# Kernel tuning notes

Measured on AMD Instinct MI355X. Metric: run time of the kernel, lower is better.

## Reference

```python
import jax, jax.numpy as jnp
import numpy as np
import math

B, S, D = 16, 512, 1024
H, L = 16, 4
DH = D // H
EPS = 1e-5


def _layernorm(x, w, b):
    mu = jnp.mean(x, axis=-1, keepdims=True)
    var = jnp.mean(jnp.square(x - mu), axis=-1, keepdims=True)
    return (x - mu) / jnp.sqrt(var + EPS) * w + b


def _pos_encoding(s, d):
    pos = jnp.arange(s, dtype=jnp.float32)[:, None]                      # [s,1]
    div = jnp.exp(jnp.arange(0, d, 2, dtype=jnp.float32) * (-math.log(10000.0) / d))
    ang = pos * div[None, :]                                             # [s,d/2]
    return jnp.stack([jnp.sin(ang), jnp.cos(ang)], axis=-1).reshape(s, d)  # interleave sin/cos


def _attention_layer(x, Wq, bq, Wv, bv, Wo, bo, gamma, ln_w, ln_b, mask):
    bs, s, d = x.shape
    # q_linear == k_linear (kq_same=True)
    q = (x @ Wq.T + bq).reshape(bs, s, H, DH).transpose(0, 2, 1, 3)      # [b,h,s,dh]
    k = q
    v = (x @ Wv.T + bv).reshape(bs, s, H, DH).transpose(0, 2, 1, 3)

    scores = jnp.einsum('bhqd,bhkd->bhqk', q, k) / math.sqrt(DH)         # [b,h,s,s]

    # distance-decay modulation (dist_scores is detached in the original)
    p = jax.nn.softmax(jnp.where(mask, scores, -1e32), axis=-1)
    distcum = jnp.cumsum(p, axis=-1)
    disttot = jnp.sum(p, axis=-1, keepdims=True)
    idx = jnp.arange(s, dtype=jnp.float32)
    pos_eff = jnp.abs(idx[None, :] - idx[:, None])[None, None, :, :]     # |i-j|
    dist = jnp.sqrt(jnp.maximum((disttot - distcum) * pos_eff, 0.0))
    dist = jax.lax.stop_gradient(dist)

    g = -jnp.abs(gamma)[None, :, None, None]                             # [1,h,1,1]
    total_effect = jnp.clip(jnp.exp(dist * g), 1e-5, 1e5)
    scores = scores * total_effect

    scores = jnp.where(mask, scores, -1e32)
    attn = jax.nn.softmax(scores, axis=-1)
    attn = jnp.where(mask, attn, 0.0)

    # maxout=True (peek_cur=False): clamp(1/max, max=5)
    scale = jnp.minimum(1.0 / jnp.max(attn, axis=-1, keepdims=True), 5.0)
    attn = attn * scale

    out = jnp.einsum('bhqk,bhkd->bhqd', attn, v)                         # [b,h,s,dh]
    out = out.transpose(0, 2, 1, 3).reshape(bs, s, d)
    out = out @ Wo.T + bo

    # eval mode: dropout = identity; residual + layernorm
    return _layernorm(x + out, ln_w, ln_b), attn


def reference(x, lens, Wq, bq, Wv, bv, Wo, bo, gammas, ln_w, ln_b, fln_w, fln_b):
    del lens  # only used in training-mode random masking
    s = x.shape[1]
    q = x + _pos_encoding(s, D)[None, :, :]
    mask = jnp.tril(jnp.ones((s, s), dtype=bool), -1)[None, None, :, :]  # peek_cur=False
    scores = None
    for l in range(L):
        q, scores = _attention_layer(q, Wq[l], bq[l], Wv[l], bv[l], Wo[l], bo[l],
                                     gammas[l], ln_w[l], ln_b[l], mask)
    return _layernorm(q, fln_w, fln_b), scores


def setup_inputs() -> dict:
    key = jax.random.key(0)
    ks = jax.random.split(key, 8)
    wscale = 1.0 / math.sqrt(D)
    return {
        'x': jax.random.normal(ks[0], (B, S, D), dtype=jnp.float32),
        'lens': jax.random.randint(ks[1], (B,), 1, S),
        'Wq': jax.random.normal(ks[2], (L, D, D), dtype=jnp.float32) * wscale,
        'bq': jnp.zeros((L, D), dtype=jnp.float32),
        'Wv': jax.random.normal(ks[3], (L, D, D), dtype=jnp.float32) * wscale,
        'bv': jnp.zeros((L, D), dtype=jnp.float32),
        'Wo': jax.random.normal(ks[4], (L, D, D), dtype=jnp.float32) * wscale,
        'bo': jnp.zeros((L, D), dtype=jnp.float32),
        'gammas': jax.random.uniform(ks[5], (L, H), dtype=jnp.float32, minval=-1.7, maxval=1.7),
        'ln_w': jnp.ones((L, D), dtype=jnp.float32),
        'ln_b': jnp.zeros((L, D), dtype=jnp.float32),
        'fln_w': jnp.ones((D,), dtype=jnp.float32),
        'fln_b': jnp.zeros((D,), dtype=jnp.float32),
    }
```

## Files before the change

kernel.cpp:

```cpp
#include <hip/hip_runtime.h>
#include <hip/hip_bf16.h>

#define BB 16
#define SS 512
#define DD 1024
#define HH 16
#define LL 4
#define DHH 64
#define GK 1024

typedef __attribute__((ext_vector_type(8))) short short8;
typedef __attribute__((ext_vector_type(4))) float f32x4;

__device__ __forceinline__ unsigned short f2bf(float f) {
  union { float f; unsigned int u; } v; v.f = f;
  unsigned int r = v.u + 0x7FFFu + ((v.u >> 16) & 1u);
  return (unsigned short)(r >> 16);
}

__device__ __forceinline__ float wave_max(float v) {
#pragma unroll
  for (int off = 32; off > 0; off >>= 1) v = fmaxf(v, __shfl_xor(v, off));
  return v;
}
__device__ __forceinline__ float wave_sum(float v) {
#pragma unroll
  for (int off = 32; off > 0; off >>= 1) v += __shfl_xor(v, off);
  return v;
}
__device__ __forceinline__ float half_max(float v) {
#pragma unroll
  for (int off = 16; off > 0; off >>= 1) v = fmaxf(v, __shfl_xor(v, off));
  return v;
}
__device__ __forceinline__ float half_sum(float v) {
#pragma unroll
  for (int off = 16; off > 0; off >>= 1) v += __shfl_xor(v, off);
  return v;
}

__device__ __forceinline__ void gl16(const void* g, void* l) {
  __builtin_amdgcn_global_load_lds(
      (const __attribute__((address_space(1))) unsigned int*)(uintptr_t)g,
      (__attribute__((address_space(3))) unsigned int*)(unsigned int)(uintptr_t)l,
      16, 0, 0);
}

__global__ __launch_bounds__(256) void k_w2bf_all(
    const float* __restrict__ wq, const float* __restrict__ wv,
    const float* __restrict__ wo, unsigned short* __restrict__ oqv,
    unsigned short* __restrict__ oo) {
  size_t i4 = ((size_t)blockIdx.x * 256 + threadIdx.x) * 4;
  const size_t QV = (size_t)2 * LL * DD * DD;
  const float* src;
  unsigned short* dst;
  if (i4 < QV) {
    size_t l = i4 >> 21;
    size_t r = i4 & ((1u << 21) - 1);
    src = (r < (1u << 20)) ? wq + (l << 20) + r
                           : wv + (l << 20) + (r - (1u << 20));
    dst = oqv + i4;
  } else {
    size_t j = i4 - QV;
    src = wo + j;
    dst = oo + j;
  }
  float4 v = *(const float4*)src;
  uint2 pk;
  pk.x = (unsigned)f2bf(v.x) | ((unsigned)f2bf(v.y) << 16);
  pk.y = (unsigned)f2bf(v.z) | ((unsigned)f2bf(v.w) << 16);
  *(uint2*)dst = pk;
}

__global__ __launch_bounds__(256) void k_add_pe(const float* __restrict__ x,
                                                float* __restrict__ out,
                                                unsigned short* __restrict__ outb) {
  size_t i4 = ((size_t)blockIdx.x * 256 + threadIdx.x) * 4;
  int d0 = (int)(i4 & (DD - 1));
  int s = (int)((i4 >> 10) & (SS - 1));
  float4 xv = *(const float4*)(x + i4);
  int ip0 = d0 >> 1;
  float f0 = __expf((float)ip0 * -0.017988946039016f);
  float f1 = __expf((float)(ip0 + 1) * -0.017988946039016f);
  float s0v, c0v, s1v, c1v;
  __sincosf((float)s * f0, &s0v, &c0v);
  __sincosf((float)s * f1, &s1v, &c1v);
  float4 o;
  o.x = xv.x + s0v; o.y = xv.y + c0v; o.z = xv.z + s1v; o.w = xv.w + c1v;
  *(float4*)(out + i4) = o;
  uint2 pk;
  pk.x = (unsigned)f2bf(o.x) | ((unsigned)f2bf(o.y) << 16);
  pk.y = (unsigned)f2bf(o.z) | ((unsigned)f2bf(o.w) << 16);
  *(uint2*)(outb + i4) = pk;
}

template <int MODE>
__global__ __launch_bounds__(256) void k_gemm(
    const unsigned short* __restrict__ A, const unsigned short* __restrict__ W,
    const float* __restrict__ bias, const float* __restrict__ bias2,
    void* __restrict__ out, void* __restrict__ out2) {
  __shared__ unsigned short As[2][128 * 32];
  __shared__ unsigned short Bs[2][128 * 32];
  const int tid = threadIdx.x;
  const int lane = tid & 63;
  const int w = tid >> 6;
  const int wr = w >> 1, wc = w & 1;
  const int fr = lane & 15, fq = lane >> 4;

  int bid = blockIdx.x;
  const int cpx = gridDim.x >> 3;
  bid = (bid & 7) * cpx + (bid >> 3);
  const int bm = (bid & 63) * 128;
  const int bn = (bid >> 6) * 128;

  f32x4 acc[4][4] = {};

  const unsigned short* ga = A + (size_t)(bm + w * 16 + (lane >> 2)) * GK + (lane & 3) * 8;
  const unsigned short* gb = W + (size_t)(bn + w * 16 + (lane >> 2)) * GK + (lane & 3) * 8;

  auto STAGE = [&](int buf, int k0) {
    unsigned short* la = As[buf] + w * 512;
    unsigned short* lb = Bs[buf] + w * 512;
    gl16(ga + k0, la);
    gl16(ga + 64 * GK + k0, la + 2048);
    gl16(gb + k0, lb);
    gl16(gb + 64 * GK + k0, lb + 2048);
  };

  STAGE(0, 0);
  __syncthreads();
  int cur = 0;
  for (int k0 = 0; k0 < GK; k0 += 32) {
    if (k0 + 32 < GK) STAGE(cur ^ 1, k0 + 32);
    short8 af[4], bf[4];
#pragma unroll
    for (int m = 0; m < 4; ++m)
      af[m] = *(const short8*)(As[cur] + (wr * 64 + m * 16 + fr) * 32 + fq * 8);
#pragma unroll
    for (int n = 0; n < 4; ++n)
      bf[n] = *(const short8*)(Bs[cur] + (wc * 64 + n * 16 + fr) * 32 + fq * 8);
#pragma unroll
    for (int m = 0; m < 4; ++m)
#pragma unroll
      for (int n = 0; n < 4; ++n)
        acc[m][n] = __builtin_amdgcn_mfma_f32_16x16x32_bf16(af[m], bf[n], acc[m][n], 0, 0, 0);
    __syncthreads();
    cur ^= 1;
  }

#pragma unroll
  for (int m = 0; m < 4; ++m) {
    const int row0 = bm + wr * 64 + m * 16 + fq * 4;
#pragma unroll
    for (int n = 0; n < 4; ++n) {
      const int col = bn + wc * 64 + n * 16 + fr;
      if constexpr (MODE == 0) {
        const float bsv = bias[col];
        unsigned short* o = (unsigned short*)out;
#pragma unroll
        for (int r = 0; r < 4; ++r)
          o[(size_t)(row0 + r) * DD + col] = f2bf(acc[m][n][r] + bsv);
      } else if constexpr (MODE == 2) {
        const float bsv = bias[col];
        float* o = (float*)out;
#pragma unroll
        for (int r = 0; r < 4; ++r)
          o[(size_t)(row0 + r) * DD + col] = acc[m][n][r] + bsv;
      } else {
        if (col < DD) {
          const float bsv = bias[col];
          unsigned short* o = (unsigned short*)out;
#pragma unroll
          for (int r = 0; r < 4; ++r)
            o[(size_t)(row0 + r) * DD + col] = f2bf(acc[m][n][r] + bsv);
        } else {
          const int c2 = col - DD;
          const float bsv = bias2[c2];
          unsigned short* o = (unsigned short*)out2;
          const int bi = row0 >> 9, si = row0 & (SS - 1);
          uint2 pk;
          pk.x = (unsigned)f2bf(acc[m][n][0] + bsv) | ((unsigned)f2bf(acc[m][n][1] + bsv) << 16);
          pk.y = (unsigned)f2bf(acc[m][n][2] + bsv) | ((unsigned)f2bf(acc[m][n][3] + bsv) << 16);
          *(uint2*)(o + ((size_t)bi * DD + c2) * SS + si) = pk;
        }
      }
    }
  }
}

__global__ __launch_bounds__(512) void k_attn(
    const unsigned short* __restrict__ Q, const unsigned short* __restrict__ Vt,
    const float* __restrict__ gam, unsigned short* __restrict__ AO,
    float* __restrict__ scores_out) {
  __shared__ float sc_s[32][516];
  __shared__ unsigned short KV[64][72];

  const int tid = threadIdx.x;
  const int lane = tid & 63;
  const int w = tid >> 6;
  const int wr = w & 1;
  const int wc = w >> 1;
  const int fr = lane & 15, fq = lane >> 4;

  const int itile = 15 - (blockIdx.x >> 8);
  const int bh = blockIdx.x & 255;
  const int b = bh >> 4;
  const int h = bh & 15;
  const int i0 = itile * 32;
  const int njt = (itile + 2) >> 1;
  const int jcap = njt * 64;

  const unsigned short* Qb = Q + (size_t)b * SS * DD + h * DHH;
  const unsigned short* Vtb = Vt + ((size_t)b * DD + h * DHH) * SS;
  const float gneg = -fabsf(gam[h]);

  const int srow = tid >> 3;
  const int sdb = (tid & 7) * 8;

  const unsigned short* qrow = Qb + (size_t)(i0 + wr * 16 + fr) * DD;
  short8 a0 = *(const short8*)(qrow + fq * 8);
  short8 a1 = *(const short8*)(qrow + 32 + fq * 8);

  short8 kreg = *(const short8*)(Qb + (size_t)srow * DD + sdb);
  for (int jt = 0; jt < njt; ++jt) {
    *(short8*)&KV[srow][sdb] = kreg;
    const unsigned short* nsrc = (jt + 1 < njt)
        ? Qb + (size_t)((jt + 1) * 64 + srow) * DD + sdb
        : Vtb + (size_t)srow * SS + sdb;
    kreg = *(const short8*)nsrc;
    __syncthreads();

    short8 b0 = *(const short8*)&KV[wc * 16 + fr][fq * 8];
    short8 b1 = *(const short8*)&KV[wc * 16 + fr][32 + fq * 8];
    f32x4 s0 = {};
    s0 = __builtin_amdgcn_mfma_f32_16x16x32_bf16(a0, b0, s0, 0, 0, 0);
    s0 = __builtin_amdgcn_mfma_f32_16x16x32_bf16(a1, b1, s0, 0, 0, 0);

    const int j = jt * 64 + wc * 16 + fr;
#pragma unroll
    for (int r = 0; r < 4; ++r) {
      const int row = wr * 16 + fq * 4 + r;
      sc_s[row][j] = (j < i0 + row) ? s0[r] * 0.125f : -1e30f;
    }
    __syncthreads();
  }
  *(short8*)&KV[srow][sdb] = kreg;

  if (itile >= 8) {
    const int jb = lane << 3;
#pragma unroll 2
    for (int q = 0; q < 4; ++q) {
      const int r_i = w * 4 + q;
      const int gi = i0 + r_i;
      const float* rowp = &sc_s[r_i][0];
      float4 v0 = *(const float4*)(rowp + jb);
      float4 v1 = *(const float4*)(rowp + jb + 4);
      float sc[8] = {v0.x, v0.y, v0.z, v0.w, v1.x, v1.y, v1.z, v1.w};
#pragma unroll
      for (int c = 0; c < 8; ++c)
        if (jb + c >= jcap) sc[c] = -1e30f;

      float p[8];
      float lsum = 0.0f;
#pragma unroll
      for (int c = 0; c < 8; ++c) {
        p[c] = __expf(sc[c]);
        lsum += p[c];
      }

      float xs = lsum;
#pragma unroll
      for (int off = 1; off < 64; off <<= 1) {
        float y = __shfl_up(xs, off);
        if (lane >= off) xs += y;
      }
      const float tot = __shfl(xs, 63);
      const float inv = 1.0f / tot;
      float run = xs - lsum;

      float s2[8];
#pragma unroll
      for (int c = 0; c < 8; ++c) {
        run += p[c];
        float cum = run * inv;
        float dist = sqrtf(fmaxf((1.0f - cum) * (float)(gi - (jb + c)), 0.0f));
        float te = __expf(gneg * dist);
        te = fminf(fmaxf(te, 1e-5f), 1e5f);
        s2[c] = sc[c] * te;
      }

      float m2 = s2[0];
#pragma unroll
      for (int c = 1; c < 8; ++c) m2 = fmaxf(m2, s2[c]);
      m2 = wave_max(m2);
      float e[8];
      float lsum2 = 0.0f;
#pragma unroll
      for (int c = 0; c < 8; ++c) {
        e[c] = __expf(s2[c] - m2);
        lsum2 += e[c];
      }
      float tot2 = wave_sum(lsum2);
      float mult = fminf(tot2, 5.0f) / tot2;

      float av[8];
#pragma unroll
      for (int c = 0; c < 8; ++c) av[c] = (gi == 0) ? 0.0f : e[c] * mult;

      if (scores_out) {
        float* so = scores_out + ((size_t)(b * HH + h) * SS + gi) * SS + jb;
        *(float4*)(so) = make_float4(av[0], av[1], av[2], av[3]);
        *(float4*)(so + 4) = make_float4(av[4], av[5], av[6], av[7]);
      }

      short8 pk;
#pragma unroll
      for (int c = 0; c < 8; ++c) pk[c] = (short)f2bf(av[c]);
      *(short8*)((unsigned short*)&sc_s[r_i][0] + jb) = pk;
    }
  } else {
    const int half = lane >> 5;
    const int ll = lane & 31;
    const int jb = ll << 3;
    for (int q = 0; q < 2; ++q) {
      const int r_i = w * 4 + q * 2 + half;
      const int gi = i0 + r_i;
      const float* rowp = &sc_s[r_i][0];
      float4 v0 = *(const float4*)(rowp + jb);
      float4 v1 = *(const float4*)(rowp + jb + 4);
      float sc[8] = {v0.x, v0.y, v0.z, v0.w, v1.x, v1.y, v1.z, v1.w};
#pragma unroll
      for (int c = 0; c < 8; ++c)
        if (jb + c >= jcap) sc[c] = -1e30f;

      float p[8];
      float lsum = 0.0f;
#pragma unroll
      for (int c = 0; c < 8; ++c) {
        p[c] = __expf(sc[c]);
        lsum += p[c];
      }

      float xs = lsum;
#pragma unroll
      for (int off = 1; off < 32; off <<= 1) {
        float y = __shfl_up(xs, off, 32);
        if (ll >= off) xs += y;
      }
      const float tot = __shfl(xs, 31, 32);
      const float inv = 1.0f / tot;
      float run = xs - lsum;

      float s2[8];
#pragma unroll
      for (int c = 0; c < 8; ++c) {
        run += p[c];
        float cum = run * inv;
        float dist = sqrtf(fmaxf((1.0f - cum) * (float)(gi - (jb + c)), 0.0f));
        float te = __expf(gneg * dist);
        te = fminf(fmaxf(te, 1e-5f), 1e5f);
        s2[c] = sc[c] * te;
      }

      float m2 = s2[0];
#pragma unroll
      for (int c = 1; c < 8; ++c) m2 = fmaxf(m2, s2[c]);
      m2 = half_max(m2);
      float e[8];
      float lsum2 = 0.0f;
#pragma unroll
      for (int c = 0; c < 8; ++c) {
        e[c] = __expf(s2[c] - m2);
        lsum2 += e[c];
      }
      const float tot2 = half_sum(lsum2);
      const float mult = fminf(tot2, 5.0f) / tot2;

      float av[8];
#pragma unroll
      for (int c = 0; c < 8; ++c) av[c] = (gi == 0) ? 0.0f : e[c] * mult;

      if (scores_out) {
        float* so = scores_out + ((size_t)(b * HH + h) * SS + gi) * SS + jb;
        *(float4*)(so) = make_float4(av[0], av[1], av[2], av[3]);
        *(float4*)(so + 4) = make_float4(av[4], av[5], av[6], av[7]);
        *(float4*)(so + 256) = make_float4(0.f, 0.f, 0.f, 0.f);
        *(float4*)(so + 260) = make_float4(0.f, 0.f, 0.f, 0.f);
      }

      short8 pk;
#pragma unroll
      for (int c = 0; c < 8; ++c) pk[c] = (short)f2bf(av[c]);
      *(short8*)((unsigned short*)&sc_s[r_i][0] + jb) = pk;
    }
  }
  __syncthreads();

  short8 vreg;
  if (njt > 1) vreg = *(const short8*)(Vtb + (size_t)srow * SS + 64 + sdb);
  f32x4 o0 = {};
  for (int jt = 0; jt < njt; ++jt) {
    const unsigned short* arow = (const unsigned short*)&sc_s[wr * 16 + fr][0];
    short8 pa0 = *(const short8*)(arow + jt * 64 + fq * 8);
    short8 pa1 = *(const short8*)(arow + jt * 64 + 32 + fq * 8);
    short8 c0 = *(const short8*)&KV[wc * 16 + fr][fq * 8];
    short8 c1 = *(const short8*)&KV[wc * 16 + fr][32 + fq * 8];
    o0 = __builtin_amdgcn_mfma_f32_16x16x32_bf16(pa0, c0, o0, 0, 0, 0);
    o0 = __builtin_amdgcn_mfma_f32_16x16x32_bf16(pa1, c1, o0, 0, 0, 0);
    __syncthreads();
    if (jt + 1 < njt) {
      *(short8*)&KV[srow][sdb] = vreg;
      if (jt + 2 < njt) vreg = *(const short8*)(Vtb + (size_t)srow * SS + (jt + 2) * 64 + sdb);
      __syncthreads();
    }
  }

  {
    const int d = h * DHH + wc * 16 + fr;
#pragma unroll
    for (int r = 0; r < 4; ++r) {
      const int row = i0 + wr * 16 + fq * 4 + r;
      AO[((size_t)b * SS + row) * DD + d] = f2bf(o0[r]);
    }
  }
}

__global__ __launch_bounds__(256) void k_res_ln(
    const float* __restrict__ x, const float* __restrict__ r,
    const float* __restrict__ w, const float* __restrict__ b,
    float* __restrict__ out, unsigned short* __restrict__ outb) {
  __shared__ float red[4];
  const int row = blockIdx.x;
  const int tid = threadIdx.x;
  const int lane = tid & 63, wv = tid >> 6;
  float4 y = ((const float4*)(x + (size_t)row * DD))[tid];
  if (r) {
    float4 rr = ((const float4*)(r + (size_t)row * DD))[tid];
    y.x += rr.x; y.y += rr.y; y.z += rr.z; y.w += rr.w;
  }
  float s = y.x + y.y + y.z + y.w;
  s = wave_sum(s);
  if (lane == 0) red[wv] = s;
  __syncthreads();
  float mean = (red[0] + red[1] + red[2] + red[3]) * (1.0f / DD);
  __syncthreads();
  float d0 = y.x - mean, d1 = y.y - mean, d2 = y.z - mean, d3 = y.w - mean;
  float s2 = d0 * d0 + d1 * d1 + d2 * d2 + d3 * d3;
  s2 = wave_sum(s2);
  if (lane == 0) red[wv] = s2;
  __syncthreads();
  float var = (red[0] + red[1] + red[2] + red[3]) * (1.0f / DD);
  float rstd = rsqrtf(var + 1e-5f);
  float4 ww = ((const float4*)w)[tid];
  float4 bb = ((const float4*)b)[tid];
  float4 o;
  o.x = d0 * rstd * ww.x + bb.x;
  o.y = d1 * rstd * ww.y + bb.y;
  o.z = d2 * rstd * ww.z + bb.z;
  o.w = d3 * rstd * ww.w + bb.w;
  ((float4*)(out + (size_t)row * DD))[tid] = o;
  if (outb) {
    uint2 pk;
    pk.x = (unsigned)f2bf(o.x) | ((unsigned)f2bf(o.y) << 16);
    pk.y = (unsigned)f2bf(o.z) | ((unsigned)f2bf(o.w) << 16);
    *(uint2*)(outb + (size_t)row * DD + tid * 4) = pk;
  }
}

extern "C" void kernel_launch(void* const* d_in, const int* in_sizes, int n_in,
                              void* d_out, int out_size, void* d_ws, size_t ws_size,
                              hipStream_t stream) {
  (void)in_sizes; (void)n_in; (void)out_size; (void)ws_size;
  const float* x = (const float*)d_in[0];
  const float* Wq = (const float*)d_in[2];
  const float* bq = (const float*)d_in[3];
  const float* Wv = (const float*)d_in[4];
  const float* bv = (const float*)d_in[5];
  const float* Wo = (const float*)d_in[6];
  const float* bo = (const float*)d_in[7];
  const float* gam = (const float*)d_in[8];
  const float* lnw = (const float*)d_in[9];
  const float* lnb = (const float*)d_in[10];
  const float* flnw = (const float*)d_in[11];
  const float* flnb = (const float*)d_in[12];

  float* out0 = (float*)d_out;
  float* scores = out0 + (size_t)BB * SS * DD;
  const size_t BUF = (size_t)BB * SS * DD;
  const size_t WSZ = (size_t)LL * DD * DD;
  const size_t BHSS = (size_t)BB * HH * SS * SS;

  float* P0 = (float*)d_ws;
  float* P1 = P0 + BUF;
  unsigned short* us = (unsigned short*)(P1 + BUF);
  unsigned short* Abf = us;
  unsigned short* Qbf = us + BUF;
  unsigned short* VtB = us + 2 * BUF;
  unsigned short* AObf = us + 3 * BUF;
  unsigned short* Wob = us + 4 * BUF;
  unsigned short* Wqvb = (unsigned short*)scores + (2 * BHSS - 2 * WSZ);

  const int M = BB * SS;

  k_w2bf_all<<<dim3(3 * WSZ / 1024), 256, 0, stream>>>(Wq, Wv, Wo, Wqvb, Wob);
  k_add_pe<<<dim3(BUF / 1024), 256, 0, stream>>>(x, P0, Abf);

  float* Acur = P0;
  float* Pnx = P1;
  for (int l = 0; l < LL; ++l) {
    float* sc_dst = (l == LL - 1) ? scores : nullptr;
    k_gemm<3><<<dim3(1024), 256, 0, stream>>>(Abf, Wqvb + (size_t)l * 2048 * DD,
                                              bq + l * DD, bv + l * DD, Qbf, VtB);
    k_attn<<<dim3(BB * HH * 16), 512, 0, stream>>>(Qbf, VtB, gam + l * HH, AObf, sc_dst);
    k_gemm<2><<<dim3(512), 256, 0, stream>>>(AObf, Wob + (size_t)l * DD * DD,
                                             bo + l * DD, nullptr, Pnx, nullptr);
    k_res_ln<<<dim3(M), 256, 0, stream>>>(Acur, Pnx, lnw + l * DD, lnb + l * DD, Pnx, Abf);
    float* t = Acur; Acur = Pnx; Pnx = t;
  }
  k_res_ln<<<dim3(M), 256, 0, stream>>>(Acur, nullptr, flnw, flnb, out0, nullptr);
}
```

Baseline: 863.4 us.

## Keep residual stream in bf16 and add MFMA priority hints in attention

```diff
diff --git a/kernel.cpp b/kernel.cpp
--- a/kernel.cpp
+++ b/kernel.cpp
@@ -16,6 +16,9 @@
   union { float f; unsigned int u; } v; v.f = f;
   unsigned int r = v.u + 0x7FFFu + ((v.u >> 16) & 1u);
   return (unsigned short)(r >> 16);
+}
+__device__ __forceinline__ float bf2f(unsigned short u) {
+  union { unsigned int i; float f; } v; v.i = ((unsigned)u) << 16; return v.f;
 }
 
 __device__ __forceinline__ float wave_max(float v) {
@@ -73,7 +76,6 @@
 }
 
 __global__ __launch_bounds__(256) void k_add_pe(const float* __restrict__ x,
-                                                float* __restrict__ out,
                                                 unsigned short* __restrict__ outb) {
   size_t i4 = ((size_t)blockIdx.x * 256 + threadIdx.x) * 4;
   int d0 = (int)(i4 & (DD - 1));
@@ -85,12 +87,10 @@
   float s0v, c0v, s1v, c1v;
   __sincosf((float)s * f0, &s0v, &c0v);
   __sincosf((float)s * f1, &s1v, &c1v);
-  float4 o;
-  o.x = xv.x + s0v; o.y = xv.y + c0v; o.z = xv.z + s1v; o.w = xv.w + c1v;
-  *(float4*)(out + i4) = o;
+  float o0 = xv.x + s0v, o1 = xv.y + c0v, o2 = xv.z + s1v, o3 = xv.w + c1v;
   uint2 pk;
-  pk.x = (unsigned)f2bf(o.x) | ((unsigned)f2bf(o.y) << 16);
-  pk.y = (unsigned)f2bf(o.z) | ((unsigned)f2bf(o.w) << 16);
+  pk.x = (unsigned)f2bf(o0) | ((unsigned)f2bf(o1) << 16);
+  pk.y = (unsigned)f2bf(o2) | ((unsigned)f2bf(o3) << 16);
   *(uint2*)(outb + i4) = pk;
 }
 
@@ -160,12 +160,6 @@
 #pragma unroll
         for (int r = 0; r < 4; ++r)
           o[(size_t)(row0 + r) * DD + col] = f2bf(acc[m][n][r] + bsv);
-      } else if constexpr (MODE == 2) {
-        const float bsv = bias[col];
-        float* o = (float*)out;
-#pragma unroll
-        for (int r = 0; r < 4; ++r)
-          o[(size_t)(row0 + r) * DD + col] = acc[m][n][r] + bsv;
       } else {
         if (col < DD) {
           const float bsv = bias[col];
@@ -233,8 +227,10 @@
     short8 b0 = *(const short8*)&KV[wc * 16 + fr][fq * 8];
     short8 b1 = *(const short8*)&KV[wc * 16 + fr][32 + fq * 8];
     f32x4 s0 = {};
+    __builtin_amdgcn_s_setprio(1);
     s0 = __builtin_amdgcn_mfma_f32_16x16x32_bf16(a0, b0, s0, 0, 0, 0);
     s0 = __builtin_amdgcn_mfma_f32_16x16x32_bf16(a1, b1, s0, 0, 0, 0);
+    __builtin_amdgcn_s_setprio(0);
 
     const int j = jt * 64 + wc * 16 + fr;
 #pragma unroll
@@ -405,8 +401,10 @@
     short8 pa1 = *(const short8*)(arow + jt * 64 + 32 + fq * 8);
     short8 c0 = *(const short8*)&KV[wc * 16 + fr][fq * 8];
     short8 c1 = *(const short8*)&KV[wc * 16 + fr][32 + fq * 8];
+    __builtin_amdgcn_s_setprio(1);
     o0 = __builtin_amdgcn_mfma_f32_16x16x32_bf16(pa0, c0, o0, 0, 0, 0);
     o0 = __builtin_amdgcn_mfma_f32_16x16x32_bf16(pa1, c1, o0, 0, 0, 0);
+    __builtin_amdgcn_s_setprio(0);
     __syncthreads();
     if (jt + 1 < njt) {
       *(short8*)&KV[srow][sdb] = vreg;
@@ -426,25 +424,32 @@
 }
 
 __global__ __launch_bounds__(256) void k_res_ln(
-    const float* __restrict__ x, const float* __restrict__ r,
+    const unsigned short* __restrict__ x, const unsigned short* __restrict__ r,
     const float* __restrict__ w, const float* __restrict__ b,
-    float* __restrict__ out, unsigned short* __restrict__ outb) {
+    unsigned short* __restrict__ outb, float* __restrict__ outf) {
   __shared__ float red[4];
   const int row = blockIdx.x;
   const int tid = threadIdx.x;
   const int lane = tid & 63, wv = tid >> 6;
-  float4 y = ((const float4*)(x + (size_t)row * DD))[tid];
+  uint2 xa = ((const uint2*)(x + (size_t)row * DD))[tid];
+  float y0 = bf2f((unsigned short)xa.x);
+  float y1 = bf2f((unsigned short)(xa.x >> 16));
+  float y2 = bf2f((unsigned short)xa.y);
+  float y3 = bf2f((unsigned short)(xa.y >> 16));
   if (r) {
-    float4 rr = ((const float4*)(r + (size_t)row * DD))[tid];
-    y.x += rr.x; y.y += rr.y; y.z += rr.z; y.w += rr.w;
-  }
-  float s = y.x + y.y + y.z + y.w;
+    uint2 ra = ((const uint2*)(r + (size_t)row * DD))[tid];
+    y0 += bf2f((unsigned short)ra.x);
+    y1 += bf2f((unsigned short)(ra.x >> 16));
+    y2 += bf2f((unsigned short)ra.y);
+    y3 += bf2f((unsigned short)(ra.y >> 16));
+  }
+  float s = y0 + y1 + y2 + y3;
   s = wave_sum(s);
   if (lane == 0) red[wv] = s;
   __syncthreads();
   float mean = (red[0] + red[1] + red[2] + red[3]) * (1.0f / DD);
   __syncthreads();
-  float d0 = y.x - mean, d1 = y.y - mean, d2 = y.z - mean, d3 = y.w - mean;
+  float d0 = y0 - mean, d1 = y1 - mean, d2 = y2 - mean, d3 = y3 - mean;
   float s2 = d0 * d0 + d1 * d1 + d2 * d2 + d3 * d3;
   s2 = wave_sum(s2);
   if (lane == 0) red[wv] = s2;
@@ -453,17 +458,17 @@
   float rstd = rsqrtf(var + 1e-5f);
   float4 ww = ((const float4*)w)[tid];
   float4 bb = ((const float4*)b)[tid];
-  float4 o;
-  o.x = d0 * rstd * ww.x + bb.x;
-  o.y = d1 * rstd * ww.y + bb.y;
-  o.z = d2 * rstd * ww.z + bb.z;
-  o.w = d3 * rstd * ww.w + bb.w;
-  ((float4*)(out + (size_t)row * DD))[tid] = o;
-  if (outb) {
+  float o0 = d0 * rstd * ww.x + bb.x;
+  float o1 = d1 * rstd * ww.y + bb.y;
+  float o2 = d2 * rstd * ww.z + bb.z;
+  float o3 = d3 * rstd * ww.w + bb.w;
+  if (outf) {
+    ((float4*)(outf + (size_t)row * DD))[tid] = make_float4(o0, o1, o2, o3);
+  } else {
     uint2 pk;
-    pk.x = (unsigned)f2bf(o.x) | ((unsigned)f2bf(o.y) << 16);
-    pk.y = (unsigned)f2bf(o.z) | ((unsigned)f2bf(o.w) << 16);
-    *(uint2*)(outb + (size_t)row * DD + tid * 4) = pk;
+    pk.x = (unsigned)f2bf(o0) | ((unsigned)f2bf(o1) << 16);
+    pk.y = (unsigned)f2bf(o2) | ((unsigned)f2bf(o3) << 16);
+    ((uint2*)(outb + (size_t)row * DD))[tid] = pk;
   }
 }
 
@@ -490,32 +495,32 @@
   const size_t WSZ = (size_t)LL * DD * DD;
   const size_t BHSS = (size_t)BB * HH * SS * SS;
 
-  float* P0 = (float*)d_ws;
-  float* P1 = P0 + BUF;
-  unsigned short* us = (unsigned short*)(P1 + BUF);
-  unsigned short* Abf = us;
-  unsigned short* Qbf = us + BUF;
-  unsigned short* VtB = us + 2 * BUF;
-  unsigned short* AObf = us + 3 * BUF;
-  unsigned short* Wob = us + 4 * BUF;
+  unsigned short* us = (unsigned short*)d_ws;
+  unsigned short* Abf0 = us;
+  unsigned short* Abf1 = us + BUF;
+  unsigned short* Qbf = us + 2 * BUF;
+  unsigned short* VtB = us + 3 * BUF;
+  unsigned short* AObf = us + 4 * BUF;
+  unsigned short* Pb = us + 5 * BUF;
+  unsigned short* Wob = us + 6 * BUF;
   unsigned short* Wqvb = (unsigned short*)scores + (2 * BHSS - 2 * WSZ);
 
   const int M = BB * SS;
 
   k_w2bf_all<<<dim3(3 * WSZ / 1024), 256, 0, stream>>>(Wq, Wv, Wo, Wqvb, Wob);
-  k_add_pe<<<dim3(BUF / 1024), 256, 0, stream>>>(x, P0, Abf);
-
-  float* Acur = P0;
-  float* Pnx = P1;
+  k_add_pe<<<dim3(BUF / 1024), 256, 0, stream>>>(x, Abf0);
+
+  unsigned short* Acur = Abf0;
+  unsigned short* Anx = Abf1;
   for (int l = 0; l < LL; ++l) {
     float* sc_dst = (l == LL - 1) ? scores : nullptr;
-    k_gemm<3><<<dim3(1024), 256, 0, stream>>>(Abf, Wqvb + (size_t)l * 2048 * DD,
+    k_gemm<3><<<dim3(1024), 256, 0, stream>>>(Acur, Wqvb + (size_t)l * 2048 * DD,
                                               bq + l * DD, bv + l * DD, Qbf, VtB);
     k_attn<<<dim3(BB * HH * 16), 512, 0, stream>>>(Qbf, VtB, gam + l * HH, AObf, sc_dst);
-    k_gemm<2><<<dim3(512), 256, 0, stream>>>(AObf, Wob + (size_t)l * DD * DD,
-                                             bo + l * DD, nullptr, Pnx, nullptr);
-    k_res_ln<<<dim3(M), 256, 0, stream>>>(Acur, Pnx, lnw + l * DD, lnb + l * DD, Pnx, Abf);
-    float* t = Acur; Acur = Pnx; Pnx = t;
-  }
-  k_res_ln<<<dim3(M), 256, 0, stream>>>(Acur, nullptr, flnw, flnb, out0, nullptr);
-}
+    k_gemm<0><<<dim3(512), 256, 0, stream>>>(AObf, Wob + (size_t)l * DD * DD,
+                                             bo + l * DD, nullptr, Pb, nullptr);
+    k_res_ln<<<dim3(M), 256, 0, stream>>>(Acur, Pb, lnw + l * DD, lnb + l * DD, Anx, nullptr);
+    unsigned short* t = Acur; Acur = Anx; Anx = t;
+  }
+  k_res_ln<<<dim3(M), 256, 0, stream>>>(Acur, nullptr, flnw, flnb, nullptr, out0);
+}
```

New measurement: 820.8 us. 4.9% less time.
